# Performance work log

Hardware: AMD Instinct MI355X
Metric: run time of the kernel (lower is better)

## Reference

```python
import jax, jax.numpy as jnp
import numpy as np

EPS_PHI = 1e-18  # weight assigned to neighbors outside the support radius


def setup_inputs() -> dict:
    key = jax.random.key(0)
    k1, k2, k3, k4 = jax.random.split(key, 4)
    N, P, K = 2, 100000, 60
    points = jax.random.normal(k1, (N, P, 3), dtype=jnp.float32)
    v = jax.random.normal(k2, (N, P, K, 3), dtype=jnp.float32)
    vn = jax.random.normal(k3, (N, P, K, 3), dtype=jnp.float32)
    # squared support radii: positive, bounded away from zero
    sr = jax.random.uniform(k4, (N, P, K), dtype=jnp.float32) + 0.1
    return {"points": points, "v": v, "vn": vn, "sr": sr}


def reference(points, v, vn, sr):
    # points: (N,P,3); v,vn: (N,P,K,3); sr: (N,P,K)
    p_v = points[:, :, None, :] - v                      # (N,P,K,3)
    dists = jnp.sum(p_v * p_v, axis=-1)                  # (N,P,K) squared distances
    inside = dists < sr                                  # (N,P,K)
    w = 1.0 - dists / sr
    phi_v = jnp.where(inside, (w * w) * (w * w), EPS_PHI)  # quartic kernel weight
    v_to_p_dot_n = jnp.sum(vn * p_v, axis=-1)            # (N,P,K)
    sdf = jnp.sum(phi_v * v_to_p_dot_n, axis=-1) / jnp.sum(phi_v, axis=-1)  # (N,P)
    return jnp.sum(sdf * sdf, axis=-1)                   # (N,)
```

## Files before the change

kernel.cpp:

```cpp
#include <hip/hip_runtime.h>

#define BT  256
#define WPB (BT / 64)
#define RED_THREADS 512
#define EPS_PHI 1e-18f

__global__ __launch_bounds__(BT, 4) void sdf_main60(
    const float* __restrict__ points,
    const float* __restrict__ v,
    const float* __restrict__ vn,
    const float* __restrict__ sr,
    float* __restrict__ ws,
    int P, int nPairs, int nWaves, int slots, int slotStride)
{
    const int lane   = threadIdx.x & 63;
    const int waveId = blockIdx.x * WPB + (threadIdx.x >> 6);
    const int g  = lane >> 4;
    const int t  = lane & 15;
    const int tc = (t < 15) ? t : 14;
    const bool act = (t < 15);

    float acc0 = 0.f, acc1 = 0.f;

    for (int pr = waveId; pr < nPairs; pr += nWaves) {
        const int pA = pr * 8 + g;
        const int pB = pA + 4;

        const float4* vA = (const float4*)(v  + (size_t)pA * 180);
        const float4* nA = (const float4*)(vn + (size_t)pA * 180);
        const float4* sA = (const float4*)(sr + (size_t)pA * 60);
        const float4* vB = (const float4*)(v  + (size_t)pB * 180);
        const float4* nB = (const float4*)(vn + (size_t)pB * 180);
        const float4* sB = (const float4*)(sr + (size_t)pB * 60);

        const float4 av0 = vA[3 * tc + 0], av1 = vA[3 * tc + 1], av2 = vA[3 * tc + 2];
        const float4 an0 = nA[3 * tc + 0], an1 = nA[3 * tc + 1], an2 = nA[3 * tc + 2];
        const float4 as4 = sA[tc];
        const float4 bv0 = vB[3 * tc + 0], bv1 = vB[3 * tc + 1], bv2 = vB[3 * tc + 2];
        const float4 bn0 = nB[3 * tc + 0], bn1 = nB[3 * tc + 1], bn2 = nB[3 * tc + 2];
        const float4 bs4 = sB[tc];
        const float pxA = points[pA * 3 + 0], pyA = points[pA * 3 + 1], pzA = points[pA * 3 + 2];
        const float pxB = points[pB * 3 + 0], pyB = points[pB * 3 + 1], pzB = points[pB * 3 + 2];

        auto quad = [&](const float4& c0, const float4& c1, const float4& c2,
                        const float4& m0, const float4& m1, const float4& m2,
                        const float4& s4, float px, float py, float pz,
                        float& num, float& den) {
            auto one = [&](float vx, float vy, float vz,
                           float nx, float ny, float nz, float s) {
                const float dx = px - vx, dy = py - vy, dz = pz - vz;
                const float d2 = dx * dx + dy * dy + dz * dz;
                const float w  = 1.f - d2 * __builtin_amdgcn_rcpf(s);
                const float w2 = w * w;
                float phi = (d2 < s) ? (w2 * w2) : EPS_PHI;
                if (!act) phi = 0.f;
                num += phi * (nx * dx + ny * dy + nz * dz);
                den += phi;
            };
            one(c0.x, c0.y, c0.z, m0.x, m0.y, m0.z, s4.x);
            one(c0.w, c1.x, c1.y, m0.w, m1.x, m1.y, s4.y);
            one(c1.z, c1.w, c2.x, m1.z, m1.w, m2.x, s4.z);
            one(c2.y, c2.z, c2.w, m2.y, m2.z, m2.w, s4.w);
        };

        float numA = 0.f, denA = 0.f, numB = 0.f, denB = 0.f;
        quad(av0, av1, av2, an0, an1, an2, as4, pxA, pyA, pzA, numA, denA);
        quad(bv0, bv1, bv2, bn0, bn1, bn2, bs4, pxB, pyB, pzB, numB, denB);

        #pragma unroll
        for (int off = 1; off <= 8; off <<= 1) {
            numA += __shfl_xor(numA, off, 64);
            denA += __shfl_xor(denA, off, 64);
            numB += __shfl_xor(numB, off, 64);
            denB += __shfl_xor(denB, off, 64);
        }

        if (t == 0) {
            const float sdfA = numA * __builtin_amdgcn_rcpf(denA);
            const float sdfB = numB * __builtin_amdgcn_rcpf(denB);
            const float sqA = sdfA * sdfA, sqB = sdfB * sdfB;
            if (pA < P) acc0 += sqA; else acc1 += sqA;
            if (pB < P) acc0 += sqB; else acc1 += sqB;
        }
    }

    #pragma unroll
    for (int off = 1; off <= 32; off <<= 1) {
        acc0 += __shfl_xor(acc0, off, 64);
        acc1 += __shfl_xor(acc1, off, 64);
    }
    if (lane == 0) {
        const int slot = waveId & (slots - 1);
        atomicAdd(&ws[slot * slotStride + 0], acc0);
        atomicAdd(&ws[slot * slotStride + 1], acc1);
    }
}

__global__ void sdf_generic(
    const float* __restrict__ points,
    const float* __restrict__ v,
    const float* __restrict__ vn,
    const float* __restrict__ sr,
    float* __restrict__ ws,
    int NP, int P, int K, int slots, int slotStride)
{
    const int p = blockIdx.x * blockDim.x + threadIdx.x;
    if (p >= NP) return;
    const float px = points[p * 3 + 0];
    const float py = points[p * 3 + 1];
    const float pz = points[p * 3 + 2];
    float num = 0.f, den = 0.f;
    for (int k = 0; k < K; ++k) {
        const size_t b = ((size_t)p * K + k) * 3;
        const float dx = px - v[b + 0];
        const float dy = py - v[b + 1];
        const float dz = pz - v[b + 2];
        const float d2 = dx * dx + dy * dy + dz * dz;
        const float s  = sr[(size_t)p * K + k];
        const float w  = 1.f - d2 / s;
        const float w2 = w * w;
        const float phi = (d2 < s) ? (w2 * w2) : EPS_PHI;
        const float dot = vn[b + 0] * dx + vn[b + 1] * dy + vn[b + 2] * dz;
        num += phi * dot;
        den += phi;
    }
    const float sdf = num / den;
    const int n = p / P;
    const int slot = p & (slots - 1);
    if (n < slotStride) atomicAdd(&ws[slot * slotStride + n], sdf * sdf);
}

__global__ __launch_bounds__(RED_THREADS) void sdf_reduce(
    const float* __restrict__ ws, float* __restrict__ out,
    int N, int slots, int slotStride)
{
    __shared__ float sm0[RED_THREADS];
    __shared__ float sm1[RED_THREADS];
    const int tid = threadIdx.x;
    float a = 0.f, b = 0.f;
    for (int s = tid; s < slots; s += RED_THREADS) {
        a += ws[s * slotStride + 0];
        if (N > 1) b += ws[s * slotStride + 1];
    }
    sm0[tid] = a;
    sm1[tid] = b;
    __syncthreads();
    #pragma unroll
    for (int s = RED_THREADS / 2; s >= 1; s >>= 1) {
        if (tid < s) {
            sm0[tid] += sm0[tid + s];
            sm1[tid] += sm1[tid + s];
        }
        __syncthreads();
    }
    if (tid == 0) {
        out[0] = sm0[0];
        if (N > 1) out[1] = sm1[0];
    }
}

extern "C" void kernel_launch(void* const* d_in, const int* in_sizes, int n_in,
                              void* d_out, int out_size, void* d_ws, size_t ws_size,
                              hipStream_t stream) {
    const float* points = (const float*)d_in[0];
    const float* v      = (const float*)d_in[1];
    const float* vn     = (const float*)d_in[2];
    const float* sr     = (const float*)d_in[3];
    float* out = (float*)d_out;
    float* ws  = (float*)d_ws;

    const int NP = in_sizes[0] / 3;
    const int K  = in_sizes[3] / NP;
    const int N  = out_size;
    const int P  = NP / N;

    int slots = 512, slotStride = 16;
    if (ws_size < (size_t)(slots * slotStride * sizeof(float))) {
        slots = 256; slotStride = 2;
    }

    hipMemsetAsync(ws, 0, (size_t)slots * slotStride * sizeof(float), stream);

    if (K == 60 && (NP & 7) == 0) {
        const int blocks = 2048;
        const int nWaves = blocks * WPB;
        const int nPairs = NP / 8;
        sdf_main60<<<blocks, BT, 0, stream>>>(points, v, vn, sr, ws,
                                              P, nPairs, nWaves,
                                              slots, slotStride);
    } else {
        sdf_generic<<<(NP + BT - 1) / BT, BT, 0, stream>>>(
            points, v, vn, sr, ws, NP, P, K, slots, slotStride);
    }
    sdf_reduce<<<1, RED_THREADS, 0, stream>>>(ws, out, N, slots, slotStride);
}
```

Baseline: 333.3 us.

## Triple-buffer neighbor data into LDS with async global-to-LDS loads

Each wave now handles groups of four points and streams their v and vn rows straight into LDS using global_load_lds. Three per-wave buffers let loads for the next two groups be in flight while the current group is computed. The sr values and point coordinates are prefetched into registers in the same rotation. Block size and grid are halved to two waves per block, and the LDS use per block rises. The code relies on the compiler inserting the right waits before LDS reads of the async loads.

```diff
diff --git a/kernel.cpp b/kernel.cpp
--- a/kernel.cpp
+++ b/kernel.cpp
@@ -1,20 +1,30 @@
 #include <hip/hip_runtime.h>
 
-#define BT  256
-#define WPB (BT / 64)
+#define BT  128
+#define WPB 2
 #define RED_THREADS 512
 #define EPS_PHI 1e-18f
 
-__global__ __launch_bounds__(BT, 4) void sdf_main60(
+#define AS1 __attribute__((address_space(1)))
+#define AS3 __attribute__((address_space(3)))
+#define GLDS(gp, lp) __builtin_amdgcn_global_load_lds( \
+    (const AS1 void*)(gp), (AS3 void*)(lp), 16, 0, 0)
+
+__global__ __launch_bounds__(BT) void sdf_main60(
     const float* __restrict__ points,
     const float* __restrict__ v,
     const float* __restrict__ vn,
     const float* __restrict__ sr,
     float* __restrict__ ws,
-    int P, int nPairs, int nWaves, int slots, int slotStride)
+    int P, int nGroups, int nWaves, int T, int slots, int slotStride)
 {
+    __shared__ float4 b0[WPB][360];
+    __shared__ float4 b1[WPB][360];
+    __shared__ float4 b2[WPB][360];
+
     const int lane   = threadIdx.x & 63;
-    const int waveId = blockIdx.x * WPB + (threadIdx.x >> 6);
+    const int w      = threadIdx.x >> 6;
+    const int waveId = blockIdx.x * WPB + w;
     const int g  = lane >> 4;
     const int t  = lane & 15;
     const int tc = (t < 15) ? t : 14;
@@ -22,67 +32,83 @@
 
     float acc0 = 0.f, acc1 = 0.f;
 
-    for (int pr = waveId; pr < nPairs; pr += nWaves) {
-        const int pA = pr * 8 + g;
-        const int pB = pA + 4;
-
-        const float4* vA = (const float4*)(v  + (size_t)pA * 180);
-        const float4* nA = (const float4*)(vn + (size_t)pA * 180);
-        const float4* sA = (const float4*)(sr + (size_t)pA * 60);
-        const float4* vB = (const float4*)(v  + (size_t)pB * 180);
-        const float4* nB = (const float4*)(vn + (size_t)pB * 180);
-        const float4* sB = (const float4*)(sr + (size_t)pB * 60);
-
-        const float4 av0 = vA[3 * tc + 0], av1 = vA[3 * tc + 1], av2 = vA[3 * tc + 2];
-        const float4 an0 = nA[3 * tc + 0], an1 = nA[3 * tc + 1], an2 = nA[3 * tc + 2];
-        const float4 as4 = sA[tc];
-        const float4 bv0 = vB[3 * tc + 0], bv1 = vB[3 * tc + 1], bv2 = vB[3 * tc + 2];
-        const float4 bn0 = nB[3 * tc + 0], bn1 = nB[3 * tc + 1], bn2 = nB[3 * tc + 2];
-        const float4 bs4 = sB[tc];
-        const float pxA = points[pA * 3 + 0], pyA = points[pA * 3 + 1], pzA = points[pA * 3 + 2];
-        const float pxB = points[pB * 3 + 0], pyB = points[pB * 3 + 1], pzB = points[pB * 3 + 2];
-
-        auto quad = [&](const float4& c0, const float4& c1, const float4& c2,
-                        const float4& m0, const float4& m1, const float4& m2,
-                        const float4& s4, float px, float py, float pz,
-                        float& num, float& den) {
-            auto one = [&](float vx, float vy, float vz,
-                           float nx, float ny, float nz, float s) {
-                const float dx = px - vx, dy = py - vy, dz = pz - vz;
-                const float d2 = dx * dx + dy * dy + dz * dz;
-                const float w  = 1.f - d2 * __builtin_amdgcn_rcpf(s);
-                const float w2 = w * w;
-                float phi = (d2 < s) ? (w2 * w2) : EPS_PHI;
-                if (!act) phi = 0.f;
-                num += phi * (nx * dx + ny * dy + nz * dz);
-                den += phi;
-            };
-            one(c0.x, c0.y, c0.z, m0.x, m0.y, m0.z, s4.x);
-            one(c0.w, c1.x, c1.y, m0.w, m1.x, m1.y, s4.y);
-            one(c1.z, c1.w, c2.x, m1.z, m1.w, m2.x, s4.z);
-            one(c2.y, c2.z, c2.w, m2.y, m2.z, m2.w, s4.w);
+    auto issue = [&](int grp, float4* lb) {
+        const float4* gv = (const float4*)(v  + (size_t)grp * 720);
+        const float4* gn = (const float4*)(vn + (size_t)grp * 720);
+        GLDS(gv +   0 + lane, lb +   0);
+        GLDS(gv +  64 + lane, lb +  64);
+        GLDS(gv + 116 + lane, lb + 116);
+        GLDS(gn +   0 + lane, lb + 180);
+        GLDS(gn +  64 + lane, lb + 244);
+        GLDS(gn + 116 + lane, lb + 296);
+    };
+    auto regs = [&](int grp, float4& s4, float& px, float& py, float& pz) {
+        const int p = grp * 4 + g;
+        s4 = ((const float4*)(sr + (size_t)p * 60))[tc];
+        px = points[p * 3 + 0];
+        py = points[p * 3 + 1];
+        pz = points[p * 3 + 2];
+    };
+    auto consume = [&](const float4* lb, int grp, const float4& s4,
+                       float px, float py, float pz) {
+        const int base = g * 45 + tc * 3;
+        const float4 c0 = lb[base + 0];
+        const float4 c1 = lb[base + 1];
+        const float4 c2 = lb[base + 2];
+        const float4 m0 = lb[180 + base + 0];
+        const float4 m1 = lb[180 + base + 1];
+        const float4 m2 = lb[180 + base + 2];
+        float num = 0.f, den = 0.f;
+        auto one = [&](float vx, float vy, float vz,
+                       float nx, float ny, float nz, float s) {
+            const float dx = px - vx, dy = py - vy, dz = pz - vz;
+            const float d2 = dx * dx + dy * dy + dz * dz;
+            const float wq = 1.f - d2 * __builtin_amdgcn_rcpf(s);
+            const float w2 = wq * wq;
+            float phi = (d2 < s) ? (w2 * w2) : EPS_PHI;
+            if (!act) phi = 0.f;
+            num += phi * (nx * dx + ny * dy + nz * dz);
+            den += phi;
         };
-
-        float numA = 0.f, denA = 0.f, numB = 0.f, denB = 0.f;
-        quad(av0, av1, av2, an0, an1, an2, as4, pxA, pyA, pzA, numA, denA);
-        quad(bv0, bv1, bv2, bn0, bn1, bn2, bs4, pxB, pyB, pzB, numB, denB);
-
+        one(c0.x, c0.y, c0.z, m0.x, m0.y, m0.z, s4.x);
+        one(c0.w, c1.x, c1.y, m0.w, m1.x, m1.y, s4.y);
+        one(c1.z, c1.w, c2.x, m1.z, m1.w, m2.x, s4.z);
+        one(c2.y, c2.z, c2.w, m2.y, m2.z, m2.w, s4.w);
         #pragma unroll
         for (int off = 1; off <= 8; off <<= 1) {
-            numA += __shfl_xor(numA, off, 64);
-            denA += __shfl_xor(denA, off, 64);
-            numB += __shfl_xor(numB, off, 64);
-            denB += __shfl_xor(denB, off, 64);
+            num += __shfl_xor(num, off, 64);
+            den += __shfl_xor(den, off, 64);
         }
-
         if (t == 0) {
-            const float sdfA = numA * __builtin_amdgcn_rcpf(denA);
-            const float sdfB = numB * __builtin_amdgcn_rcpf(denB);
-            const float sqA = sdfA * sdfA, sqB = sdfB * sdfB;
-            if (pA < P) acc0 += sqA; else acc1 += sqA;
-            if (pB < P) acc0 += sqB; else acc1 += sqB;
+            const float sdf = num * __builtin_amdgcn_rcpf(den);
+            const float sq  = sdf * sdf;
+            if (grp * 4 + g < P) acc0 += sq; else acc1 += sq;
         }
-    }
+    };
+
+    const int j0 = waveId;
+    float4 s0 = {0,0,0,0}, s1 = {0,0,0,0}, s2 = {0,0,0,0};
+    float px0=0, py0=0, pz0=0, px1=0, py1=0, pz1=0, px2=0, py2=0, pz2=0;
+
+    if (j0 < nGroups)          { issue(j0, b0[w]);          regs(j0, s0, px0, py0, pz0); }
+    if (j0 + nWaves < nGroups) { issue(j0 + nWaves, b1[w]); regs(j0 + nWaves, s1, px1, py1, pz1); }
+
+    #define STEP(BC, BI, sC, pxC, pyC, pzC, sI, pxI, pyI, pzI)               \
+    {                                                                         \
+        const int cons = j0 + it * nWaves;                                    \
+        const int nxt  = cons + 2 * nWaves;                                   \
+        if (nxt < nGroups)  { issue(nxt, BI); regs(nxt, sI, pxI, pyI, pzI); } \
+        if (cons < nGroups) consume(BC, cons, sC, pxC, pyC, pzC);             \
+        ++it;                                                                 \
+    }
+
+    int it = 0;
+    while (it < T) {
+        STEP(b0[w], b2[w], s0, px0, py0, pz0, s2, px2, py2, pz2)
+        if (it < T) STEP(b1[w], b0[w], s1, px1, py1, pz1, s0, px0, py0, pz0)
+        if (it < T) STEP(b2[w], b1[w], s2, px2, py2, pz2, s1, px1, py1, pz1)
+    }
+    #undef STEP
 
     #pragma unroll
     for (int off = 1; off <= 32; off <<= 1) {
@@ -181,15 +207,16 @@
 
     hipMemsetAsync(ws, 0, (size_t)slots * slotStride * sizeof(float), stream);
 
-    if (K == 60 && (NP & 7) == 0) {
-        const int blocks = 2048;
-        const int nWaves = blocks * WPB;
-        const int nPairs = NP / 8;
+    if (K == 60 && (NP & 3) == 0) {
+        const int blocks  = 1024;
+        const int nWaves  = blocks * WPB;
+        const int nGroups = NP / 4;
+        const int T       = (nGroups + nWaves - 1) / nWaves;
         sdf_main60<<<blocks, BT, 0, stream>>>(points, v, vn, sr, ws,
-                                              P, nPairs, nWaves,
+                                              P, nGroups, nWaves, T,
                                               slots, slotStride);
     } else {
-        sdf_generic<<<(NP + BT - 1) / BT, BT, 0, stream>>>(
+        sdf_generic<<<(NP + 255) / 256, 256, 0, stream>>>(
             points, v, vn, sr, ws, NP, P, K, slots, slotStride);
     }
     sdf_reduce<<<1, RED_THREADS, 0, stream>>>(ws, out, N, slots, slotStride);
```

Result: no change. 330.7 us (-0.8%).
